# Optimization experiments

Measured on AMD Instinct MI355X. Metric: run time of the kernel, lower is better.

The kernel has to match this reference:

```python
import jax, jax.numpy as jnp
import numpy as np


def _conv1d_same(x, w, b):
    # x: (B, Cin, T), w: (Cout, Cin, K) -> (B, Cout, T)
    y = jax.lax.conv_general_dilated(x, w, window_strides=(1,), padding='SAME',
                                     dimension_numbers=('NCH', 'OIH', 'NCH'))
    return y + b[None, :, None]


def _deform_conv1d(x, offsets, w, b):
    # x: (B, C, T); offsets: (B, K, T) per-tap fractional offsets;
    # w: (Cout, Cin, K); linear interpolation, zero padding outside [0, T-1].
    B, C, T = x.shape
    K = w.shape[-1]
    center = (K - 1) // 2
    taps = (jnp.arange(K) - center).astype(x.dtype)                 # (K,)
    t = jnp.arange(T, dtype=x.dtype)                                # (T,)
    pos = t[None, None, :] + taps[None, :, None] + offsets          # (B, K, T)
    p0 = jnp.floor(pos)
    frac = pos - p0                                                 # (B, K, T)
    p0i = p0.astype(jnp.int32)

    def gather(idx):
        valid = ((idx >= 0) & (idx < T)).astype(x.dtype)            # (B, K, T)
        idxc = jnp.clip(idx, 0, T - 1)
        g = jnp.take_along_axis(
            jnp.broadcast_to(x[:, :, None, :], (B, C, K, T)),
            jnp.broadcast_to(idxc[:, None, :, :], (B, C, K, T)), axis=3)
        return g * valid[:, None, :, :]

    sampled = gather(p0i) * (1.0 - frac)[:, None] + gather(p0i + 1) * frac[:, None]  # (B,C,K,T)
    return jnp.einsum('bckt,ock->bot', sampled, w) + b[None, :, None]


def _align_level(x, mask, off, params):
    # Two stacked PackedDeformConv1d layers: offset conv predicts per-tap
    # offsets which are accumulated with the incoming offsets, then the
    # deformable conv samples x at the offset positions; relu + mask gate.
    for (w, bias, ow, ob) in params:
        off = _conv1d_same(x, ow, ob) + off
        x = jax.nn.relu(_deform_conv1d(x, off, w, bias)) * mask
    return x, off


def setup_inputs() -> dict:
    key = jax.random.key(0)
    ks = jax.random.split(key, 16)
    B, C, K = 8, 512, 3
    Ts = [2048, 1024, 512]
    d = {}
    for i, T in enumerate(Ts):
        d[f'feats_{i}'] = jax.random.normal(ks[i], (B, C, T), jnp.float32)
        d[f'mask_{i}'] = jnp.ones((B, 1, T), jnp.float32)
        d[f'offs_{i}'] = jax.random.normal(ks[3 + i], (B, K, T), jnp.float32)
    for l in range(2):
        d[f'w{l}'] = jax.random.normal(ks[6 + 2 * l], (C, C, K), jnp.float32) * 0.01
        d[f'b{l}'] = jnp.zeros((C,), jnp.float32)
        d[f'ow{l}'] = jax.random.normal(ks[7 + 2 * l], (K, C, K), jnp.float32) * 0.1
        d[f'ob{l}'] = jnp.zeros((K,), jnp.float32)
    return d


def reference(feats_0, feats_1, feats_2, mask_0, mask_1, mask_2,
              offs_0, offs_1, offs_2, w0, b0, ow0, ob0, w1, b1, ow1, ob1):
    params = [(w0, b0, ow0, ob0), (w1, b1, ow1, ob1)]
    feats = (feats_0, feats_1, feats_2)
    masks = (mask_0, mask_1, mask_2)
    offs = (offs_0, offs_1, offs_2)
    outs, new_masks = [], []
    for x, m, off in zip(feats, masks, offs):
        y, _ = _align_level(x, m, off, params)
        outs.append(y)
        new_masks.append(m.astype(bool))
    return tuple(outs) + tuple(new_masks)
```

## Files before the change

kernel.cpp:

```cpp
#include <hip/hip_runtime.h>
#include <hip/hip_bf16.h>
#include <stdint.h>

typedef __attribute__((ext_vector_type(8))) short bf16x8;
typedef __attribute__((ext_vector_type(4))) short bf16x4;
typedef __attribute__((ext_vector_type(4))) float f32x4;

__device__ __forceinline__ float b2f(short s) {
  union { unsigned u; float f; } cv;
  cv.u = ((unsigned)(unsigned short)s) << 16;
  return cv.f;
}
__device__ __forceinline__ short f2b(float f) {
  __hip_bfloat16 h = __float2bfloat16(f);
  return *reinterpret_cast<short*>(&h);
}


__global__ __launch_bounds__(256) void setup_kernel(
    const float* __restrict__ w0, const float* __restrict__ w1,
    __hip_bfloat16* __restrict__ d0, __hip_bfloat16* __restrict__ d1,
    const float* __restrict__ ow1,
    __hip_bfloat16* __restrict__ of1hi, __hip_bfloat16* __restrict__ of1lo,
    const float* __restrict__ m0, const float* __restrict__ m1, const float* __restrict__ m2,
    float* __restrict__ mo) {
  int i = blockIdx.x * 256 + threadIdx.x;
  if (i < 1572864) {
    int l = i >= 786432;
    int i2 = i - (l ? 786432 : 0);
    const float* w = l ? w1 : w0;
    __hip_bfloat16* d = l ? d1 : d0;
    int fid = i2 >> 9, within = i2 & 511, lane = within >> 3, j = within & 7;
    int mb = fid / 48, kt = fid - mb * 48;
    int o = mb * 16 + (lane & 15);
    int r = kt * 32 + (lane >> 4) * 8 + j;
    int k = r >> 9, c = r & 511;
    d[i2] = __float2bfloat16(w[o * 1536 + c * 3 + k]);
  } else if (i < 1597440) {
    int i4 = i - 1572864;
    int fid = i4 >> 9, within = i4 & 511, lane = within >> 3, jj = within & 7;
    int o = lane & 15;
    int rr = fid * 32 + (lane >> 4) * 8 + jj;
    int j = rr >> 9, c = rr & 511;
    float v = (o < 3) ? ow1[o * 1536 + c * 3 + j] : 0.f;
    __hip_bfloat16 hi = __float2bfloat16(v);
    of1hi[i4] = hi;
    of1lo[i4] = __float2bfloat16(v - __bfloat162float(hi));
  } else {
    int i2 = i - 1597440;
    if (i2 < 28672) {
      float v;
      if (i2 < 16384) v = m0[i2];
      else if (i2 < 24576) v = m1[i2 - 16384];
      else v = m2[i2 - 24576];
      mo[i2] = (v != 0.f) ? 1.f : 0.f;
    }
  }
}

__global__ __launch_bounds__(256) void transpose_kernel(const float* __restrict__ x0,
                                                        const float* __restrict__ x1,
                                                        const float* __restrict__ x2,
                                                        __hip_bfloat16* __restrict__ xT) {
  __shared__ float fl[64][65];
  int f = blockIdx.x;
  int lv = (f < 2048) ? 0 : ((f < 3072) ? 1 : 2);
  int f2 = f - ((lv == 0) ? 0 : ((lv == 1) ? 2048 : 3072));
  int tsh = 11 - lv;
  const float* x = (lv == 0) ? x0 : ((lv == 1) ? x1 : x2);
  __hip_bfloat16* xo = xT + ((lv == 0) ? 0 : ((lv == 1) ? 8388608 : 12582912));
  int perb = (1 << (tsh - 6)) * 8;
  int b = f2 / perb;
  int rem = f2 - b * perb;
  int t0 = (rem >> 3) << 6;
  int c0 = (rem & 7) << 6;
  int tid = threadIdx.x;
  int tl = tid & 63, cw = tid >> 6;
  const float* xb = x + ((size_t)(b * 512 + c0) << tsh) + t0;
#pragma unroll
  for (int i = 0; i < 16; ++i) {
    int cl = cw + i * 4;
    fl[cl][tl] = xb[((size_t)cl << tsh) + tl];
  }
  __syncthreads();
  int tl2 = tid >> 2;
  int cb = (tid & 3) << 4;
  short* orow = (short*)xo + (((size_t)(b << tsh) + t0 + tl2) << 9) + c0 + cb;
#pragma unroll
  for (int h = 0; h < 2; ++h) {
    bf16x8 v;
#pragma unroll
    for (int j = 0; j < 8; ++j) v[j] = f2b(fl[cb + h * 8 + j][tl2]);
    *(bf16x8*)(orow + h * 8) = v;
  }
}

__global__ __launch_bounds__(256) void offconv1_kernel(const float* __restrict__ x0p,
                                                       const float* __restrict__ x1p,
                                                       const float* __restrict__ x2p,
                                                       const float* __restrict__ ow,
                                                       float* __restrict__ P) {
  __shared__ float red[3][4][64];
  int tid = threadIdx.x, lane = tid & 63, w = tid >> 6;
  int bx = blockIdx.x;
  int lv = (bx < 256) ? 0 : ((bx < 384) ? 1 : 2);
  int lbx = bx - ((lv == 0) ? 0 : ((lv == 1) ? 256 : 384));
  int tsh = 11 - lv;
  int T = 1 << tsh;
  const float* x = (lv == 0) ? x0p : ((lv == 1) ? x1p : x2p);
  float* Pl = P + ((lv == 0) ? 0 : ((lv == 1) ? 196608 : 294912));
  int nchunk = T >> 6;
  int b = lbx >> (tsh - 6);
  int tb = (lbx & (nchunk - 1)) << 6;
  int t = tb + lane;
  int c0 = blockIdx.y * 128 + w * 32;
  const float* xb = x + ((size_t)(b * 512 + c0) << tsh);
  float a0 = 0.f, a1 = 0.f, a2 = 0.f;
  for (int c = 0; c < 32; ++c) {
    const float* xr = xb + ((size_t)c << tsh);
    float xm = (t > 0) ? xr[t - 1] : 0.f;
    float x0 = xr[t];
    float xp = (t < T - 1) ? xr[t + 1] : 0.f;
    const float* wp = ow + (c0 + c) * 3;
    a0 += wp[0] * xm + wp[1] * x0 + wp[2] * xp;
    a1 += wp[1536] * xm + wp[1537] * x0 + wp[1538] * xp;
    a2 += wp[3072] * xm + wp[3073] * x0 + wp[3074] * xp;
  }
  red[0][w][lane] = a0;
  red[1][w][lane] = a1;
  red[2][w][lane] = a2;
  __syncthreads();
  if (w < 3) {
    float s = red[w][0][lane] + red[w][1][lane] + red[w][2][lane] + red[w][3][lane];
    Pl[blockIdx.y * (24 << tsh) + ((b * 3 + w) << tsh) + tb + lane] = s;
  }
}

__global__ __launch_bounds__(256, 4) void offconv2_kernel(const __hip_bfloat16* __restrict__ xT,
                                                          const __hip_bfloat16* __restrict__ oHi,
                                                          const __hip_bfloat16* __restrict__ oLo,
                                                          float* __restrict__ offc) {
  int tid = threadIdx.x, lane = tid & 63, wid = tid >> 6;
  int nt = blockIdx.x * 4 + wid;
  int lv = (nt < 1024) ? 0 : ((nt < 1536) ? 1 : 2);
  int ntl = nt - ((lv == 0) ? 0 : ((lv == 1) ? 1024 : 1536));
  int tsh = 11 - lv;
  int T = 1 << tsh;
  const short* xp = (const short*)xT + ((lv == 0) ? 0 : ((lv == 1) ? 8388608 : 12582912));
  float* oc = offc + ((lv == 0) ? 0 : ((lv == 1) ? 49152 : 73728));
  int n = (ntl << 4) + (lane & 15);
  int b = n >> tsh;
  int t = n & (T - 1);
  const short* hip_ = (const short*)oHi + lane * 8;
  const short* lop_ = (const short*)oLo + lane * 8;
  int co = (lane >> 4) << 3;
  f32x4 acc = {};
  for (int kt = 0; kt < 48; ++kt) {
    int j = kt >> 4;
    int c0 = ((kt & 15) << 5) + co;
    int row = t + j - 1;
    bf16x8 bv = {};
    if ((unsigned)row < (unsigned)T)
      bv = *(const bf16x8*)(xp + (((size_t)(b << tsh) + row) << 9) + c0);
    bf16x8 ah = *(const bf16x8*)(hip_ + ((size_t)kt << 9));
    bf16x8 al = *(const bf16x8*)(lop_ + ((size_t)kt << 9));
    acc = __builtin_amdgcn_mfma_f32_16x16x32_bf16(ah, bv, acc, 0, 0, 0);
    acc = __builtin_amdgcn_mfma_f32_16x16x32_bf16(al, bv, acc, 0, 0, 0);
  }
  if ((lane >> 4) == 0) {
#pragma unroll
    for (int r = 0; r < 3; ++r) oc[((b * 3 + r) << tsh) + t] = acc[r];
  }
}

template <bool LAYER2, bool OUT_BF16>
__global__ __launch_bounds__(256, 3) void dgemm_kernel(
    const __hip_bfloat16* __restrict__ xT, const __hip_bfloat16* __restrict__ Wf,
    const float* __restrict__ off0, const float* __restrict__ off1,
    const float* __restrict__ off2, const float* __restrict__ P1,
    const float* __restrict__ offc2, const float* __restrict__ ob0v,
    const float* __restrict__ ob1v, const float* __restrict__ bias,
    const float* __restrict__ mk0, const float* __restrict__ mk1, const float* __restrict__ mk2,
    void* __restrict__ o0, void* __restrict__ o1, void* __restrict__ o2) {
  __shared__ short sS[2][2048];
  __shared__ float s_f[3][64];
  __shared__ int s_q0[3][64];
  int tid = threadIdx.x, lane = tid & 63, wid = tid >> 6;
  int bx = blockIdx.x;
  int lv = (bx < 256) ? 0 : ((bx < 384) ? 1 : 2);
  int lbx = bx - ((lv == 0) ? 0 : ((lv == 1) ? 256 : 384));
  int tsh = 11 - lv;
  int T = 1 << tsh;
  const short* xp = (const short*)xT + ((lv == 0) ? 0 : ((lv == 1) ? 8388608 : 12582912));
  const float* offin = (lv == 0) ? off0 : ((lv == 1) ? off1 : off2);
  const float* P1l = P1 + ((lv == 0) ? 0 : ((lv == 1) ? 196608 : 294912));
  const float* oc2 = offc2 + ((lv == 0) ? 0 : ((lv == 1) ? 49152 : 73728));
  const float* mask = (lv == 0) ? mk0 : ((lv == 1) ? mk1 : mk2);
  void* outp = (lv == 0) ? o0 : ((lv == 1) ? o1 : o2);
  int nchunk = T >> 6;
  int b = lbx >> (tsh - 6);
  int tb = (lbx & (nchunk - 1)) << 6;
  int mhalf = blockIdx.y;

  if (tid < 192) {
    int k = tid >> 6, tl = tid & 63, t = tb + tl;
    int oi = ((b * 3 + k) << tsh) + t;
    int PT = 24 << tsh;
    float o = offin[oi] + ob0v[k];
    o += P1l[oi] + P1l[PT + oi] + P1l[2 * PT + oi] + P1l[3 * PT + oi];
    if (LAYER2) o += ob1v[k] + oc2[oi];
    float pos = (float)(t + k - 1) + o;
    float pf = floorf(pos);
    s_f[k][tl] = pos - pf;
    s_q0[k][tl] = (int)pf;
  }
  __syncthreads();

  f32x4 acc[4][4] = {};
  int gtl = (wid << 4) + (lane & 15);
  const short* wfp = (const short*)Wf + (size_t)(mhalf * 16 + wid * 4) * 48 * 512 + lane * 8;
  int buf = 0;
  for (int k3 = 0; k3 < 3; ++k3) {
    int q0 = s_q0[k3][gtl];
    float f = s_f[k3][gtl];
    bool ok0 = (unsigned)q0 < (unsigned)T;
    bool ok1 = (unsigned)(q0 + 1) < (unsigned)T;
    const short* r0p = xp + (((size_t)(b << tsh) + q0) << 9) + ((lane >> 4) << 3);
#pragma unroll 4
    for (int kk = 0; kk < 16; ++kk) {
      int kt = k3 * 16 + kk;
      bf16x8 v0 = {}, v1 = {};
      if (ok0) v0 = *(const bf16x8*)(r0p + (kk << 5));
      if (ok1) v1 = *(const bf16x8*)(r0p + 512 + (kk << 5));
      bf16x8 ov;
#pragma unroll
      for (int j = 0; j < 8; ++j) {
        float a = b2f(v0[j]);
        ov[j] = f2b(a + (b2f(v1[j]) - a) * f);
      }
      *(bf16x8*)&sS[buf][(wid << 9) + lane * 8] = ov;
      __syncthreads();
      bf16x8 av[4], bv[4];
#pragma unroll
      for (int i = 0; i < 4; ++i)
        av[i] = *(const bf16x8*)(wfp + ((size_t)(i * 48 + kt) << 9));
#pragma unroll
      for (int jj = 0; jj < 4; ++jj) bv[jj] = *(const bf16x8*)&sS[buf][(jj << 9) + lane * 8];
#pragma unroll
      for (int i = 0; i < 4; ++i)
#pragma unroll
        for (int jj = 0; jj < 4; ++jj)
          acc[i][jj] = __builtin_amdgcn_mfma_f32_16x16x32_bf16(av[i], bv[jj], acc[i][jj], 0, 0, 0);
      buf ^= 1;
    }
  }

  int lrow = lane & 15, lq = lane >> 4;
  int mbase = mhalf * 256 + wid * 64;
  float bvals[4][4];
#pragma unroll
  for (int i = 0; i < 4; ++i)
#pragma unroll
    for (int r = 0; r < 4; ++r) bvals[i][r] = bias[mbase + i * 16 + lq * 4 + r];
#pragma unroll
  for (int j = 0; j < 4; ++j) {
    int col = j * 16 + lrow;
    int t = tb + col;
    float mk = mask[(b << tsh) + t];
    if (OUT_BF16) {
      short* orow = (short*)outp + (((size_t)(b << tsh) + t) << 9);
#pragma unroll
      for (int i = 0; i < 4; ++i) {
        bf16x4 pv;
#pragma unroll
        for (int r = 0; r < 4; ++r)
          pv[r] = f2b(fmaxf(acc[i][j][r] + bvals[i][r], 0.f) * mk);
        *(bf16x4*)(orow + mbase + i * 16 + lq * 4) = pv;
      }
    } else {
#pragma unroll
      for (int i = 0; i < 4; ++i) {
        int m = mbase + i * 16 + lq * 4;
#pragma unroll
        for (int r = 0; r < 4; ++r) {
          float v = fmaxf(acc[i][j][r] + bvals[i][r], 0.f) * mk;
          ((float*)outp)[(((size_t)(b * 512 + m + r)) << tsh) + t] = v;
        }
      }
    }
  }
}

extern "C" void kernel_launch(void* const* d_in, const int* in_sizes, int n_in, void* d_out,
                              int out_size, void* d_ws, size_t ws_size, hipStream_t stream) {
  const float* feats[3] = {(const float*)d_in[0], (const float*)d_in[3], (const float*)d_in[6]};
  const float* maskp[3] = {(const float*)d_in[1], (const float*)d_in[4], (const float*)d_in[7]};
  const float* offs[3] = {(const float*)d_in[2], (const float*)d_in[5], (const float*)d_in[8]};
  const float* w[2] = {(const float*)d_in[9], (const float*)d_in[13]};
  const float* bias[2] = {(const float*)d_in[10], (const float*)d_in[14]};
  const float* ow[2] = {(const float*)d_in[11], (const float*)d_in[15]};
  const float* ob[2] = {(const float*)d_in[12], (const float*)d_in[16]};

  const size_t YOFF[3] = {0, 8388608, 12582912};
  const size_t MOFF = 14680064;

  uint8_t* ws = (uint8_t*)d_ws;
  __hip_bfloat16* Wf0 = (__hip_bfloat16*)ws;
  __hip_bfloat16* Wf1 = (__hip_bfloat16*)(ws + 1572864);
  __hip_bfloat16* owF1hi = (__hip_bfloat16*)(ws + 3145728);
  __hip_bfloat16* owF1lo = (__hip_bfloat16*)(ws + 3194880);
  float* P1 = (float*)(ws + 3244032);
  float* offc2 = (float*)(ws + 4620288);
  __hip_bfloat16* fT = (__hip_bfloat16*)(ws + 8388608);
  __hip_bfloat16* x1T = (__hip_bfloat16*)(ws + 37748736);

  float* outf = (float*)d_out;

  setup_kernel<<<6448, 256, 0, stream>>>(w[0], w[1], Wf0, Wf1, ow[1], owF1hi, owF1lo,
                                         maskp[0], maskp[1], maskp[2], outf + MOFF);
  transpose_kernel<<<3584, 256, 0, stream>>>(feats[0], feats[1], feats[2], fT);
  offconv1_kernel<<<dim3(448, 4), 256, 0, stream>>>(feats[0], feats[1], feats[2], ow[0], P1);

  dgemm_kernel<false, true><<<dim3(448, 2), 256, 0, stream>>>(
      fT, Wf0, offs[0], offs[1], offs[2], P1, offc2, ob[0], ob[1], bias[0],
      maskp[0], maskp[1], maskp[2], (void*)x1T, (void*)(x1T + YOFF[1]), (void*)(x1T + YOFF[2]));

  offconv2_kernel<<<448, 256, 0, stream>>>(x1T, owF1hi, owF1lo, offc2);
  dgemm_kernel<true, false><<<dim3(448, 2), 256, 0, stream>>>(
      x1T, Wf1, offs[0], offs[1], offs[2], P1, offc2, ob[0], ob[1], bias[1],
      maskp[0], maskp[1], maskp[2], (void*)(outf + YOFF[0]), (void*)(outf + YOFF[1]),
      (void*)(outf + YOFF[2]));
}
```

Measured before the change: 352.8 us.

## Fuse first offset conv into transpose and software-pipeline deformable GEMM loads

The first-layer offset convolution now runs inside the transpose kernel, reusing the tile already staged in shared memory plus halo columns. This removes a separate pass over the fp32 features, and the partial sums are split 8 ways across channel groups instead of 4. The deformable GEMM loop is fully unrolled with register prefetch of the next step's gathered rows and weight fragments. A bare waitcnt+barrier replaces __syncthreads. The trade-off is higher register pressure and a larger partial-sum buffer that the GEMM has to reduce.

```diff
diff --git a/kernel.cpp b/kernel.cpp
--- a/kernel.cpp
+++ b/kernel.cpp
@@ -58,17 +58,23 @@
   }
 }
 
-__global__ __launch_bounds__(256) void transpose_kernel(const float* __restrict__ x0,
-                                                        const float* __restrict__ x1,
-                                                        const float* __restrict__ x2,
-                                                        __hip_bfloat16* __restrict__ xT) {
+__global__ __launch_bounds__(256) void tconv_kernel(const float* __restrict__ x0,
+                                                    const float* __restrict__ x1,
+                                                    const float* __restrict__ x2,
+                                                    const float* __restrict__ ow,
+                                                    __hip_bfloat16* __restrict__ xT,
+                                                    float* __restrict__ P) {
   __shared__ float fl[64][65];
+  __shared__ float fl2[64][2];
+  __shared__ float red[3][4][64];
   int f = blockIdx.x;
   int lv = (f < 2048) ? 0 : ((f < 3072) ? 1 : 2);
   int f2 = f - ((lv == 0) ? 0 : ((lv == 1) ? 2048 : 3072));
   int tsh = 11 - lv;
+  int T = 1 << tsh;
   const float* x = (lv == 0) ? x0 : ((lv == 1) ? x1 : x2);
   __hip_bfloat16* xo = xT + ((lv == 0) ? 0 : ((lv == 1) ? 8388608 : 12582912));
+  float* Pl = P + ((lv == 0) ? 0 : ((lv == 1) ? 393216 : 589824));
   int perb = (1 << (tsh - 6)) * 8;
   int b = f2 / perb;
   int rem = f2 - b * perb;
@@ -82,57 +88,49 @@
     int cl = cw + i * 4;
     fl[cl][tl] = xb[((size_t)cl << tsh) + tl];
   }
+  if (tid < 128) {
+    int c = tid & 63, side = tid >> 6;
+    int tg = side ? (t0 + 64) : (t0 - 1);
+    float v = 0.f;
+    if ((unsigned)tg < (unsigned)T) v = x[((size_t)(b * 512 + c0 + c) << tsh) + tg];
+    fl2[c][side] = v;
+  }
   __syncthreads();
-  int tl2 = tid >> 2;
-  int cb = (tid & 3) << 4;
-  short* orow = (short*)xo + (((size_t)(b << tsh) + t0 + tl2) << 9) + c0 + cb;
-#pragma unroll
-  for (int h = 0; h < 2; ++h) {
-    bf16x8 v;
-#pragma unroll
-    for (int j = 0; j < 8; ++j) v[j] = f2b(fl[cb + h * 8 + j][tl2]);
-    *(bf16x8*)(orow + h * 8) = v;
-  }
-}
-
-__global__ __launch_bounds__(256) void offconv1_kernel(const float* __restrict__ x0p,
-                                                       const float* __restrict__ x1p,
-                                                       const float* __restrict__ x2p,
-                                                       const float* __restrict__ ow,
-                                                       float* __restrict__ P) {
-  __shared__ float red[3][4][64];
-  int tid = threadIdx.x, lane = tid & 63, w = tid >> 6;
-  int bx = blockIdx.x;
-  int lv = (bx < 256) ? 0 : ((bx < 384) ? 1 : 2);
-  int lbx = bx - ((lv == 0) ? 0 : ((lv == 1) ? 256 : 384));
-  int tsh = 11 - lv;
-  int T = 1 << tsh;
-  const float* x = (lv == 0) ? x0p : ((lv == 1) ? x1p : x2p);
-  float* Pl = P + ((lv == 0) ? 0 : ((lv == 1) ? 196608 : 294912));
-  int nchunk = T >> 6;
-  int b = lbx >> (tsh - 6);
-  int tb = (lbx & (nchunk - 1)) << 6;
-  int t = tb + lane;
-  int c0 = blockIdx.y * 128 + w * 32;
-  const float* xb = x + ((size_t)(b * 512 + c0) << tsh);
-  float a0 = 0.f, a1 = 0.f, a2 = 0.f;
-  for (int c = 0; c < 32; ++c) {
-    const float* xr = xb + ((size_t)c << tsh);
-    float xm = (t > 0) ? xr[t - 1] : 0.f;
-    float x0 = xr[t];
-    float xp = (t < T - 1) ? xr[t + 1] : 0.f;
-    const float* wp = ow + (c0 + c) * 3;
-    a0 += wp[0] * xm + wp[1] * x0 + wp[2] * xp;
-    a1 += wp[1536] * xm + wp[1537] * x0 + wp[1538] * xp;
-    a2 += wp[3072] * xm + wp[3073] * x0 + wp[3074] * xp;
-  }
-  red[0][w][lane] = a0;
-  red[1][w][lane] = a1;
-  red[2][w][lane] = a2;
+  {
+    int tl2 = tid >> 2;
+    int cb = (tid & 3) << 4;
+    short* orow = (short*)xo + (((size_t)(b << tsh) + t0 + tl2) << 9) + c0 + cb;
+#pragma unroll
+    for (int h = 0; h < 2; ++h) {
+      bf16x8 v;
+#pragma unroll
+      for (int j = 0; j < 8; ++j) v[j] = f2b(fl[cb + h * 8 + j][tl2]);
+      *(bf16x8*)(orow + h * 8) = v;
+    }
+  }
+  {
+    int t = tid & 63, cq = tid >> 6;
+    float a0 = 0.f, a1 = 0.f, a2 = 0.f;
+#pragma unroll
+    for (int c2 = 0; c2 < 16; ++c2) {
+      int c = cq * 16 + c2;
+      float xm = (t > 0) ? fl[c][t - 1] : fl2[c][0];
+      float x0v = fl[c][t];
+      float xp = (t < 63) ? fl[c][t + 1] : fl2[c][1];
+      const float* wp = ow + (c0 + c) * 3;
+      a0 += wp[0] * xm + wp[1] * x0v + wp[2] * xp;
+      a1 += wp[1536] * xm + wp[1537] * x0v + wp[1538] * xp;
+      a2 += wp[3072] * xm + wp[3073] * x0v + wp[3074] * xp;
+    }
+    red[0][cq][t] = a0;
+    red[1][cq][t] = a1;
+    red[2][cq][t] = a2;
+  }
   __syncthreads();
-  if (w < 3) {
-    float s = red[w][0][lane] + red[w][1][lane] + red[w][2][lane] + red[w][3][lane];
-    Pl[blockIdx.y * (24 << tsh) + ((b * 3 + w) << tsh) + tb + lane] = s;
+  if (tid < 192) {
+    int k = tid >> 6, t = tid & 63;
+    float s = red[k][0][t] + red[k][1][t] + red[k][2][t] + red[k][3][t];
+    Pl[(c0 >> 6) * (24 << tsh) + ((b * 3 + k) << tsh) + t0 + t] = s;
   }
 }
 
@@ -177,7 +175,7 @@
 __global__ __launch_bounds__(256, 3) void dgemm_kernel(
     const __hip_bfloat16* __restrict__ xT, const __hip_bfloat16* __restrict__ Wf,
     const float* __restrict__ off0, const float* __restrict__ off1,
-    const float* __restrict__ off2, const float* __restrict__ P1,
+    const float* __restrict__ off2, const float* __restrict__ P8,
     const float* __restrict__ offc2, const float* __restrict__ ob0v,
     const float* __restrict__ ob1v, const float* __restrict__ bias,
     const float* __restrict__ mk0, const float* __restrict__ mk1, const float* __restrict__ mk2,
@@ -193,7 +191,7 @@
   int T = 1 << tsh;
   const short* xp = (const short*)xT + ((lv == 0) ? 0 : ((lv == 1) ? 8388608 : 12582912));
   const float* offin = (lv == 0) ? off0 : ((lv == 1) ? off1 : off2);
-  const float* P1l = P1 + ((lv == 0) ? 0 : ((lv == 1) ? 196608 : 294912));
+  const float* P8l = P8 + ((lv == 0) ? 0 : ((lv == 1) ? 393216 : 589824));
   const float* oc2 = offc2 + ((lv == 0) ? 0 : ((lv == 1) ? 49152 : 73728));
   const float* mask = (lv == 0) ? mk0 : ((lv == 1) ? mk1 : mk2);
   void* outp = (lv == 0) ? o0 : ((lv == 1) ? o1 : o2);
@@ -207,7 +205,8 @@
     int oi = ((b * 3 + k) << tsh) + t;
     int PT = 24 << tsh;
     float o = offin[oi] + ob0v[k];
-    o += P1l[oi] + P1l[PT + oi] + P1l[2 * PT + oi] + P1l[3 * PT + oi];
+#pragma unroll
+    for (int g = 0; g < 8; ++g) o += P8l[g * PT + oi];
     if (LAYER2) o += ob1v[k] + oc2[oi];
     float pos = (float)(t + k - 1) + o;
     float pf = floorf(pos);
@@ -216,43 +215,65 @@
   }
   __syncthreads();
 
+  int gtl = (wid << 4) + (lane & 15);
+  int q0r[3];
+  float fr[3];
+  bool ok0[3], ok1[3];
+  const short* rp[3];
+#pragma unroll
+  for (int k = 0; k < 3; ++k) {
+    q0r[k] = s_q0[k][gtl];
+    fr[k] = s_f[k][gtl];
+    ok0[k] = (unsigned)q0r[k] < (unsigned)T;
+    ok1[k] = (unsigned)(q0r[k] + 1) < (unsigned)T;
+    rp[k] = xp + ((ptrdiff_t)((b << tsh) + q0r[k]) << 9) + ((lane >> 4) << 3);
+  }
+  const short* wfp = (const short*)Wf + (size_t)(mhalf * 16 + wid * 4) * 48 * 512 + lane * 8;
+
   f32x4 acc[4][4] = {};
-  int gtl = (wid << 4) + (lane & 15);
-  const short* wfp = (const short*)Wf + (size_t)(mhalf * 16 + wid * 4) * 48 * 512 + lane * 8;
+  bf16x8 v0 = {}, v1 = {}, av[4];
+  if (ok0[0]) v0 = *(const bf16x8*)rp[0];
+  if (ok1[0]) v1 = *(const bf16x8*)(rp[0] + 512);
+#pragma unroll
+  for (int i = 0; i < 4; ++i) av[i] = *(const bf16x8*)(wfp + ((size_t)(i * 48) << 9));
+
   int buf = 0;
-  for (int k3 = 0; k3 < 3; ++k3) {
-    int q0 = s_q0[k3][gtl];
-    float f = s_f[k3][gtl];
-    bool ok0 = (unsigned)q0 < (unsigned)T;
-    bool ok1 = (unsigned)(q0 + 1) < (unsigned)T;
-    const short* r0p = xp + (((size_t)(b << tsh) + q0) << 9) + ((lane >> 4) << 3);
-#pragma unroll 4
-    for (int kk = 0; kk < 16; ++kk) {
-      int kt = k3 * 16 + kk;
-      bf16x8 v0 = {}, v1 = {};
-      if (ok0) v0 = *(const bf16x8*)(r0p + (kk << 5));
-      if (ok1) v1 = *(const bf16x8*)(r0p + 512 + (kk << 5));
-      bf16x8 ov;
-#pragma unroll
-      for (int j = 0; j < 8; ++j) {
-        float a = b2f(v0[j]);
-        ov[j] = f2b(a + (b2f(v1[j]) - a) * f);
-      }
-      *(bf16x8*)&sS[buf][(wid << 9) + lane * 8] = ov;
-      __syncthreads();
-      bf16x8 av[4], bv[4];
-#pragma unroll
-      for (int i = 0; i < 4; ++i)
-        av[i] = *(const bf16x8*)(wfp + ((size_t)(i * 48 + kt) << 9));
-#pragma unroll
-      for (int jj = 0; jj < 4; ++jj) bv[jj] = *(const bf16x8*)&sS[buf][(jj << 9) + lane * 8];
-#pragma unroll
-      for (int i = 0; i < 4; ++i)
-#pragma unroll
-        for (int jj = 0; jj < 4; ++jj)
-          acc[i][jj] = __builtin_amdgcn_mfma_f32_16x16x32_bf16(av[i], bv[jj], acc[i][jj], 0, 0, 0);
-      buf ^= 1;
-    }
+#pragma unroll
+  for (int kt = 0; kt < 48; ++kt) {
+    float f = fr[kt >> 4];
+    bf16x8 ov;
+#pragma unroll
+    for (int j = 0; j < 8; ++j) {
+      float a = b2f(v0[j]);
+      ov[j] = f2b(a + (b2f(v1[j]) - a) * f);
+    }
+    bf16x8 nv0 = {}, nv1 = {}, nav[4];
+    if (kt < 47) {
+      int n = kt + 1, k3 = n >> 4, kk = n & 15;
+      const short* a = rp[k3] + (kk << 5);
+      if (ok0[k3]) nv0 = *(const bf16x8*)a;
+      if (ok1[k3]) nv1 = *(const bf16x8*)(a + 512);
+#pragma unroll
+      for (int i = 0; i < 4; ++i) nav[i] = *(const bf16x8*)(wfp + ((size_t)(i * 48 + n) << 9));
+    } else {
+#pragma unroll
+      for (int i = 0; i < 4; ++i) nav[i] = av[i];
+    }
+    *(bf16x8*)&sS[buf][(wid << 9) + lane * 8] = ov;
+    asm volatile("s_waitcnt lgkmcnt(0)\n\ts_barrier" ::: "memory");
+    bf16x8 bv[4];
+#pragma unroll
+    for (int j = 0; j < 4; ++j) bv[j] = *(const bf16x8*)&sS[buf][(j << 9) + lane * 8];
+#pragma unroll
+    for (int i = 0; i < 4; ++i)
+#pragma unroll
+      for (int j = 0; j < 4; ++j)
+        acc[i][j] = __builtin_amdgcn_mfma_f32_16x16x32_bf16(av[i], bv[j], acc[i][j], 0, 0, 0);
+    v0 = nv0;
+    v1 = nv1;
+#pragma unroll
+    for (int i = 0; i < 4; ++i) av[i] = nav[i];
+    buf ^= 1;
   }
 
   int lrow = lane & 15, lq = lane >> 4;
@@ -309,8 +330,8 @@
   __hip_bfloat16* Wf1 = (__hip_bfloat16*)(ws + 1572864);
   __hip_bfloat16* owF1hi = (__hip_bfloat16*)(ws + 3145728);
   __hip_bfloat16* owF1lo = (__hip_bfloat16*)(ws + 3194880);
-  float* P1 = (float*)(ws + 3244032);
-  float* offc2 = (float*)(ws + 4620288);
+  float* P8 = (float*)(ws + 3244032);
+  float* offc2 = (float*)(ws + 5996544);
   __hip_bfloat16* fT = (__hip_bfloat16*)(ws + 8388608);
   __hip_bfloat16* x1T = (__hip_bfloat16*)(ws + 37748736);
 
@@ -318,16 +339,15 @@
 
   setup_kernel<<<6448, 256, 0, stream>>>(w[0], w[1], Wf0, Wf1, ow[1], owF1hi, owF1lo,
                                          maskp[0], maskp[1], maskp[2], outf + MOFF);
-  transpose_kernel<<<3584, 256, 0, stream>>>(feats[0], feats[1], feats[2], fT);
-  offconv1_kernel<<<dim3(448, 4), 256, 0, stream>>>(feats[0], feats[1], feats[2], ow[0], P1);
+  tconv_kernel<<<3584, 256, 0, stream>>>(feats[0], feats[1], feats[2], ow[0], fT, P8);
 
   dgemm_kernel<false, true><<<dim3(448, 2), 256, 0, stream>>>(
-      fT, Wf0, offs[0], offs[1], offs[2], P1, offc2, ob[0], ob[1], bias[0],
+      fT, Wf0, offs[0], offs[1], offs[2], P8, offc2, ob[0], ob[1], bias[0],
       maskp[0], maskp[1], maskp[2], (void*)x1T, (void*)(x1T + YOFF[1]), (void*)(x1T + YOFF[2]));
 
   offconv2_kernel<<<448, 256, 0, stream>>>(x1T, owF1hi, owF1lo, offc2);
   dgemm_kernel<true, false><<<dim3(448, 2), 256, 0, stream>>>(
-      x1T, Wf1, offs[0], offs[1], offs[2], P1, offc2, ob[0], ob[1], bias[1],
+      x1T, Wf1, offs[0], offs[1], offs[2], P8, offc2, ob[0], ob[1], bias[1],
       maskp[0], maskp[1], maskp[2], (void*)(outf + YOFF[0]), (void*)(outf + YOFF[1]),
       (void*)(outf + YOFF[2]));
 }
```

After: 415.6 us. +17.8%, slower.
